# Kernel tuning notes

Measured on AMD Instinct MI355X. Metric: run time of the kernel, lower is better.

The kernel has to match this reference:

```python
import jax, jax.numpy as jnp
import numpy as np

OUT, IN = 4096, 4096  # W_shape
K, BLOCK = 256, 8     # codebook entries, block dim


def setup_inputs() -> dict:
    key = jax.random.key(0)
    k1, k2, k3, k4, k5 = jax.random.split(key, 5)
    x = jax.random.normal(k1, (4, 2048, IN), dtype=jnp.float32)
    centroids = jax.random.normal(k2, (K, BLOCK), dtype=jnp.float32)
    labels = jax.random.randint(k3, (OUT * IN // BLOCK,), 0, K, dtype=jnp.int64)
    scale = jax.random.uniform(k4, (IN,), dtype=jnp.float32)
    bias = jax.random.normal(k5, (OUT,), dtype=jnp.float32)
    return {"x": x, "centroids": centroids, "labels": labels, "scale": scale, "bias": bias}


def reference(x, centroids, labels, scale, bias):
    # VQ weight decompression: gather codebook vectors, reshape to [OUT, IN]
    W_smooth = centroids[labels].reshape(OUT, IN)
    # F.linear(x * scale, W, bias) == (x*scale) @ W.T + bias
    return jnp.einsum('bsi,oi->bso', x * scale, W_smooth) + bias
```

## Files before the change

kernel.cpp:

```cpp
#include <hip/hip_runtime.h>
#include <stdint.h>

#define M_DIM 8192
#define N_DIM 4096
#define K_DIM 4096
#define NUM_VQ (N_DIM * K_DIM / 8)
#define NUM_X  (M_DIM * K_DIM)
#define VQ_BLOCKS (NUM_VQ / 256)
#define CVT_BLOCKS (NUM_X / 8 / 256)

#define DEPTH  4
#define TILES  (K_DIM / 32)
#define ROUNDS (TILES / DEPTH)

#define AS1 __attribute__((address_space(1)))
#define AS3 __attribute__((address_space(3)))

typedef __attribute__((ext_vector_type(4))) float f32x4;
typedef __attribute__((ext_vector_type(8))) short bf16x8;
typedef unsigned short u16;

__device__ inline unsigned short f2bf(float f) {
    union { float f; unsigned int i; } v; v.f = f;
    unsigned int x = v.i;
    return (unsigned short)((x + 0x7FFFu + ((x >> 16) & 1u)) >> 16);
}

__global__ void prep(const int* __restrict__ labels,
                     const float* __restrict__ centroids,
                     const float* __restrict__ scale,
                     const float* __restrict__ x,
                     u16* __restrict__ Ws, u16* __restrict__ Xb) {
    int b = blockIdx.x;
    if (b < VQ_BLOCKS) {
        int lane = threadIdx.x & 63;
        int probe = labels[2 * lane + 1];
        bool is64 = (__ballot(probe != 0) == 0ull);
        int i = b * 256 + threadIdx.x;
        int lab = is64 ? labels[2 * i] : labels[i];
        int kb = i & 511;
        f32x4 c0 = ((const f32x4*)centroids)[2 * lab];
        f32x4 c1 = ((const f32x4*)centroids)[2 * lab + 1];
        f32x4 s0 = ((const f32x4*)scale)[2 * kb];
        f32x4 s1 = ((const f32x4*)scale)[2 * kb + 1];
        bf16x8 o;
#pragma unroll
        for (int j = 0; j < 4; ++j) {
            o[j]     = (short)f2bf(c0[j] * s0[j]);
            o[4 + j] = (short)f2bf(c1[j] * s1[j]);
        }
        ((bf16x8*)Ws)[i] = o;
    } else {
        int i = (b - VQ_BLOCKS) * 256 + threadIdx.x;
        f32x4 a = ((const f32x4*)x)[2 * i];
        f32x4 c = ((const f32x4*)x)[2 * i + 1];
        bf16x8 o;
#pragma unroll
        for (int j = 0; j < 4; ++j) { o[j] = (short)f2bf(a[j]); o[4 + j] = (short)f2bf(c[j]); }
        ((bf16x8*)Xb)[i] = o;
    }
}

__global__ __launch_bounds__(512, 4)
void gemm_bias(const u16* __restrict__ A, const u16* __restrict__ B,
               const float* __restrict__ bias, float* __restrict__ C) {
    __shared__ u16 buf[DEPTH * 8192];
    __shared__ int ready[DEPTH];
    __shared__ int done[DEPTH];

    const int tid  = threadIdx.x;
    const int wave = tid >> 6;
    const int lane = tid & 63;
    const int bm = blockIdx.y * 128;
    const int bn = blockIdx.x * 128;

    if (tid < DEPTH) done[tid] = 0;
    else if (tid < 2 * DEPTH) ready[tid - DEPTH] = 0;
    __syncthreads();

    if (wave >= 4) {
        const int s = wave - 4;
        u16* stA = buf + s * 8192;
        u16* stB = stA + 4096;
        const int prow = lane >> 2;
        const int scol = (((lane & 3) ^ ((lane >> 3) & 3))) * 8;
        const u16* baseA = A + (size_t)(bm + prow) * K_DIM + scol;
        const u16* baseB = B + (size_t)(bn + prow) * K_DIM + scol;

        for (int r = 0; r < ROUNDS; ++r) {
            const int kt = r * DEPTH + s;
            while (__hip_atomic_load(&done[s], __ATOMIC_ACQUIRE,
                                     __HIP_MEMORY_SCOPE_WORKGROUP) < 4 * r)
                __builtin_amdgcn_s_sleep(1);
            const u16* gA = baseA + kt * 32;
            const u16* gB = baseB + kt * 32;
#pragma unroll
            for (int j = 0; j < 8; ++j)
                __builtin_amdgcn_global_load_lds(
                    (const AS1 void*)(gA + (size_t)(16 * j) * K_DIM),
                    (AS3 void*)(stA + j * 512), 16, 0, 0);
#pragma unroll
            for (int j = 0; j < 8; ++j)
                __builtin_amdgcn_global_load_lds(
                    (const AS1 void*)(gB + (size_t)(16 * j) * K_DIM),
                    (AS3 void*)(stB + j * 512), 16, 0, 0);
            asm volatile("s_waitcnt vmcnt(0)" ::: "memory");
            __hip_atomic_store(&ready[s], r + 1, __ATOMIC_RELEASE,
                               __HIP_MEMORY_SCOPE_WORKGROUP);
        }
        return;
    }

    const int wm = (wave >> 1) * 64;
    const int wn = (wave & 1) * 64;
    const int fm = lane & 15;
    const int fks = (((lane >> 4) ^ ((lane >> 1) & 3)) & 3) * 8;

    f32x4 acc[4][4];
#pragma unroll
    for (int i = 0; i < 4; ++i)
#pragma unroll
        for (int j = 0; j < 4; ++j)
            acc[i][j] = (f32x4){0.f, 0.f, 0.f, 0.f};

    for (int kt = 0; kt < TILES; ++kt) {
        const int s = kt & (DEPTH - 1);
        const int r = kt >> 2;
        while (__hip_atomic_load(&ready[s], __ATOMIC_ACQUIRE,
                                 __HIP_MEMORY_SCOPE_WORKGROUP) < r + 1)
            __builtin_amdgcn_s_sleep(1);
        const u16* stA = buf + s * 8192;
        const u16* stB = stA + 4096;

        bf16x8 af[4], bfr[4];
#pragma unroll
        for (int i = 0; i < 4; ++i)
            af[i] = *(const bf16x8*)&stA[(wm + i * 16 + fm) * 32 + fks];
#pragma unroll
        for (int j = 0; j < 4; ++j)
            bfr[j] = *(const bf16x8*)&stB[(wn + j * 16 + fm) * 32 + fks];

        if (lane == 0)
            __hip_atomic_fetch_add(&done[s], 1, __ATOMIC_RELEASE,
                                   __HIP_MEMORY_SCOPE_WORKGROUP);

#pragma unroll
        for (int i = 0; i < 4; ++i)
#pragma unroll
            for (int j = 0; j < 4; ++j)
                acc[i][j] = __builtin_amdgcn_mfma_f32_16x16x32_bf16(
                    af[i], bfr[j], acc[i][j], 0, 0, 0);
    }

    float biasv[4];
#pragma unroll
    for (int j = 0; j < 4; ++j)
        biasv[j] = bias[bn + wn + j * 16 + (lane & 15)];

    const int crow0 = bm + wm + (lane >> 4) * 4;
    const int ccol0 = bn + wn + (lane & 15);
#pragma unroll
    for (int i = 0; i < 4; ++i)
#pragma unroll
        for (int r = 0; r < 4; ++r) {
            size_t rowoff = (size_t)(crow0 + i * 16 + r) * N_DIM;
#pragma unroll
            for (int j = 0; j < 4; ++j)
                C[rowoff + ccol0 + j * 16] = acc[i][j][r] + biasv[j];
        }
}

extern "C" void kernel_launch(void* const* d_in, const int* in_sizes, int n_in,
                              void* d_out, int out_size, void* d_ws, size_t ws_size,
                              hipStream_t stream) {
    const float* x         = (const float*)d_in[0];
    const float* centroids = (const float*)d_in[1];
    const int*   labels    = (const int*)d_in[2];
    const float* scale     = (const float*)d_in[3];
    const float* bias      = (const float*)d_in[4];
    float* out             = (float*)d_out;

    u16* Ws = (u16*)d_ws;
    u16* Xb = (u16*)((char*)d_ws + (size_t)NUM_VQ * 16);

    prep<<<VQ_BLOCKS + CVT_BLOCKS, 256, 0, stream>>>(labels, centroids, scale, x,
                                                     Ws, Xb);

    dim3 grid(N_DIM / 128, M_DIM / 128);
    gemm_bias<<<grid, 512, 0, stream>>>(Xb, Ws, bias, out);
}
```

Baseline: 534.8 us.

## Double K tile to 64 with two-stage producer pipeline and split prep kernels

The GEMM now loads K tiles of 64 instead of 32 into two LDS stages instead of four, with two producer waves instead of four (384 threads per block). The LDS swizzle is reworked for 64-column rows and each consumer wave issues two MFMAs per fragment pair per tile. This halves the number of producer/consumer handshakes and spin-waits per K step and gives more MFMA work per synchronisation. The cost is less prefetch depth and possibly lower occupancy. The fused prep kernel is also split into separate weight and activation conversion kernels.

```diff
diff --git a/kernel.cpp b/kernel.cpp
--- a/kernel.cpp
+++ b/kernel.cpp
@@ -9,8 +9,9 @@
 #define VQ_BLOCKS (NUM_VQ / 256)
 #define CVT_BLOCKS (NUM_X / 8 / 256)
 
-#define DEPTH  4
-#define TILES  (K_DIM / 32)
+#define BK     64
+#define DEPTH  2
+#define TILES  (K_DIM / BK)
 #define ROUNDS (TILES / DEPTH)
 
 #define AS1 __attribute__((address_space(1)))
@@ -26,45 +27,43 @@
     return (unsigned short)((x + 0x7FFFu + ((x >> 16) & 1u)) >> 16);
 }
 
-__global__ void prep(const int* __restrict__ labels,
-                     const float* __restrict__ centroids,
-                     const float* __restrict__ scale,
-                     const float* __restrict__ x,
-                     u16* __restrict__ Ws, u16* __restrict__ Xb) {
-    int b = blockIdx.x;
-    if (b < VQ_BLOCKS) {
-        int lane = threadIdx.x & 63;
-        int probe = labels[2 * lane + 1];
-        bool is64 = (__ballot(probe != 0) == 0ull);
-        int i = b * 256 + threadIdx.x;
-        int lab = is64 ? labels[2 * i] : labels[i];
-        int kb = i & 511;
-        f32x4 c0 = ((const f32x4*)centroids)[2 * lab];
-        f32x4 c1 = ((const f32x4*)centroids)[2 * lab + 1];
-        f32x4 s0 = ((const f32x4*)scale)[2 * kb];
-        f32x4 s1 = ((const f32x4*)scale)[2 * kb + 1];
-        bf16x8 o;
+__global__ void prep_w(const int* __restrict__ labels,
+                       const float* __restrict__ centroids,
+                       const float* __restrict__ scale,
+                       u16* __restrict__ Ws) {
+    int lane = threadIdx.x & 63;
+    int probe = labels[2 * lane + 1];
+    bool is64 = (__ballot(probe != 0) == 0ull);
+    int i = blockIdx.x * 256 + threadIdx.x;
+    int lab = is64 ? labels[2 * i] : labels[i];
+    int kb = i & 511;
+    f32x4 c0 = ((const f32x4*)centroids)[2 * lab];
+    f32x4 c1 = ((const f32x4*)centroids)[2 * lab + 1];
+    f32x4 s0 = ((const f32x4*)scale)[2 * kb];
+    f32x4 s1 = ((const f32x4*)scale)[2 * kb + 1];
+    bf16x8 o;
 #pragma unroll
-        for (int j = 0; j < 4; ++j) {
-            o[j]     = (short)f2bf(c0[j] * s0[j]);
-            o[4 + j] = (short)f2bf(c1[j] * s1[j]);
-        }
-        ((bf16x8*)Ws)[i] = o;
-    } else {
-        int i = (b - VQ_BLOCKS) * 256 + threadIdx.x;
-        f32x4 a = ((const f32x4*)x)[2 * i];
-        f32x4 c = ((const f32x4*)x)[2 * i + 1];
-        bf16x8 o;
-#pragma unroll
-        for (int j = 0; j < 4; ++j) { o[j] = (short)f2bf(a[j]); o[4 + j] = (short)f2bf(c[j]); }
-        ((bf16x8*)Xb)[i] = o;
+    for (int j = 0; j < 4; ++j) {
+        o[j]     = (short)f2bf(c0[j] * s0[j]);
+        o[4 + j] = (short)f2bf(c1[j] * s1[j]);
     }
+    ((bf16x8*)Ws)[i] = o;
 }
 
-__global__ __launch_bounds__(512, 4)
+__global__ void prep_x(const float* __restrict__ x, u16* __restrict__ Xb) {
+    int i = blockIdx.x * 256 + threadIdx.x;
+    f32x4 a = ((const f32x4*)x)[2 * i];
+    f32x4 c = ((const f32x4*)x)[2 * i + 1];
+    bf16x8 o;
+#pragma unroll
+    for (int j = 0; j < 4; ++j) { o[j] = (short)f2bf(a[j]); o[4 + j] = (short)f2bf(c[j]); }
+    ((bf16x8*)Xb)[i] = o;
+}
+
+__global__ __launch_bounds__(384, 3)
 void gemm_bias(const u16* __restrict__ A, const u16* __restrict__ B,
                const float* __restrict__ bias, float* __restrict__ C) {
-    __shared__ u16 buf[DEPTH * 8192];
+    __shared__ u16 buf[DEPTH * 16384];
     __shared__ int ready[DEPTH];
     __shared__ int done[DEPTH];
 
@@ -80,10 +79,10 @@
 
     if (wave >= 4) {
         const int s = wave - 4;
-        u16* stA = buf + s * 8192;
-        u16* stB = stA + 4096;
-        const int prow = lane >> 2;
-        const int scol = (((lane & 3) ^ ((lane >> 3) & 3))) * 8;
+        u16* stA = buf + s * 16384;
+        u16* stB = stA + 8192;
+        const int prow = lane >> 3;
+        const int scol = ((lane & 7) ^ prow) * 8;
         const u16* baseA = A + (size_t)(bm + prow) * K_DIM + scol;
         const u16* baseB = B + (size_t)(bn + prow) * K_DIM + scol;
 
@@ -92,17 +91,17 @@
             while (__hip_atomic_load(&done[s], __ATOMIC_ACQUIRE,
                                      __HIP_MEMORY_SCOPE_WORKGROUP) < 4 * r)
                 __builtin_amdgcn_s_sleep(1);
-            const u16* gA = baseA + kt * 32;
-            const u16* gB = baseB + kt * 32;
+            const u16* gA = baseA + kt * BK;
+            const u16* gB = baseB + kt * BK;
 #pragma unroll
-            for (int j = 0; j < 8; ++j)
+            for (int j = 0; j < 16; ++j)
                 __builtin_amdgcn_global_load_lds(
-                    (const AS1 void*)(gA + (size_t)(16 * j) * K_DIM),
+                    (const AS1 void*)(gA + (size_t)(8 * j) * K_DIM),
                     (AS3 void*)(stA + j * 512), 16, 0, 0);
 #pragma unroll
-            for (int j = 0; j < 8; ++j)
+            for (int j = 0; j < 16; ++j)
                 __builtin_amdgcn_global_load_lds(
-                    (const AS1 void*)(gB + (size_t)(16 * j) * K_DIM),
+                    (const AS1 void*)(gB + (size_t)(8 * j) * K_DIM),
                     (AS3 void*)(stB + j * 512), 16, 0, 0);
             asm volatile("s_waitcnt vmcnt(0)" ::: "memory");
             __hip_atomic_store(&ready[s], r + 1, __ATOMIC_RELEASE,
@@ -114,7 +113,8 @@
     const int wm = (wave >> 1) * 64;
     const int wn = (wave & 1) * 64;
     const int fm = lane & 15;
-    const int fks = (((lane >> 4) ^ ((lane >> 1) & 3)) & 3) * 8;
+    const int pc0 = (((lane >> 4)    ) ^ (lane & 7)) * 8;
+    const int pc1 = (((lane >> 4) | 4) ^ (lane & 7)) * 8;
 
     f32x4 acc[4][4];
 #pragma unroll
@@ -125,20 +125,24 @@
 
     for (int kt = 0; kt < TILES; ++kt) {
         const int s = kt & (DEPTH - 1);
-        const int r = kt >> 2;
+        const int r = kt >> 1;
         while (__hip_atomic_load(&ready[s], __ATOMIC_ACQUIRE,
                                  __HIP_MEMORY_SCOPE_WORKGROUP) < r + 1)
             __builtin_amdgcn_s_sleep(1);
-        const u16* stA = buf + s * 8192;
-        const u16* stB = stA + 4096;
+        const u16* stA = buf + s * 16384;
+        const u16* stB = stA + 8192;
 
-        bf16x8 af[4], bfr[4];
+        bf16x8 a0[4], b0[4], a1[4], b1[4];
 #pragma unroll
-        for (int i = 0; i < 4; ++i)
-            af[i] = *(const bf16x8*)&stA[(wm + i * 16 + fm) * 32 + fks];
+        for (int i = 0; i < 4; ++i) {
+            a0[i] = *(const bf16x8*)&stA[(wm + i * 16 + fm) * 64 + pc0];
+            a1[i] = *(const bf16x8*)&stA[(wm + i * 16 + fm) * 64 + pc1];
+        }
 #pragma unroll
-        for (int j = 0; j < 4; ++j)
-            bfr[j] = *(const bf16x8*)&stB[(wn + j * 16 + fm) * 32 + fks];
+        for (int j = 0; j < 4; ++j) {
+            b0[j] = *(const bf16x8*)&stB[(wn + j * 16 + fm) * 64 + pc0];
+            b1[j] = *(const bf16x8*)&stB[(wn + j * 16 + fm) * 64 + pc1];
+        }
 
         if (lane == 0)
             __hip_atomic_fetch_add(&done[s], 1, __ATOMIC_RELEASE,
@@ -147,9 +151,12 @@
 #pragma unroll
         for (int i = 0; i < 4; ++i)
 #pragma unroll
-            for (int j = 0; j < 4; ++j)
+            for (int j = 0; j < 4; ++j) {
                 acc[i][j] = __builtin_amdgcn_mfma_f32_16x16x32_bf16(
-                    af[i], bfr[j], acc[i][j], 0, 0, 0);
+                    a0[i], b0[j], acc[i][j], 0, 0, 0);
+                acc[i][j] = __builtin_amdgcn_mfma_f32_16x16x32_bf16(
+                    a1[i], b1[j], acc[i][j], 0, 0, 0);
+            }
     }
 
     float biasv[4];
@@ -183,9 +190,9 @@
     u16* Ws = (u16*)d_ws;
     u16* Xb = (u16*)((char*)d_ws + (size_t)NUM_VQ * 16);
 
-    prep<<<VQ_BLOCKS + CVT_BLOCKS, 256, 0, stream>>>(labels, centroids, scale, x,
-                                                     Ws, Xb);
+    prep_w<<<VQ_BLOCKS, 256, 0, stream>>>(labels, centroids, scale, Ws);
+    prep_x<<<CVT_BLOCKS, 256, 0, stream>>>(x, Xb);
 
     dim3 grid(N_DIM / 128, M_DIM / 128);
-    gemm_bias<<<grid, 512, 0, stream>>>(Xb, Ws, bias, out);
+    gemm_bias<<<grid, 384, 0, stream>>>(Xb, Ws, bias, out);
 }
```

Result: faster. 520.9 us (-2.6%).
